# Performance work log

Measured on AMD Instinct MI355X. Metric: run time of the kernel, lower is better.

Reference implementation:

```python
import jax, jax.numpy as jnp
import numpy as np

IN, H = 24, 128


def _lstm_last(x, W_ih, W_hh, b_ih, b_hh):
    # x: [B, T, IN]. PyTorch gate order: i, f, g, o. Returns final hidden state [B, H].
    B = x.shape[0]
    b = b_ih + b_hh  # [4H]
    # Precompute input projections for all timesteps: [T, B, 4H]
    xg = jnp.einsum('bti,gi->tbg', x, W_ih) + b

    def step(carry, xg_t):
        h, c = carry
        gates = xg_t + h @ W_hh.T  # [B, 4H]
        i, f, g, o = jnp.split(gates, 4, axis=-1)
        i = jax.nn.sigmoid(i)
        f = jax.nn.sigmoid(f)
        g = jnp.tanh(g)
        o = jax.nn.sigmoid(o)
        c = f * c + i * g
        h = o * jnp.tanh(c)
        return (h, c), None

    h0 = jnp.zeros((B, H), x.dtype)
    (h, _), _ = jax.lax.scan(step, (h0, h0), xg)
    return h


def setup_inputs() -> dict:
    key = jax.random.key(0)
    ks = jax.random.split(key, 10)
    s_ih = 1.0 / np.sqrt(H)
    return {
        'x': jax.random.normal(ks[0], (1024, 512, IN), jnp.float32),
        'additional_input': jax.random.normal(ks[1], (1024, 2), jnp.float32),
        'W_ih': jax.random.uniform(ks[2], (4 * H, IN), jnp.float32, -s_ih, s_ih),
        'W_hh': jax.random.uniform(ks[3], (4 * H, H), jnp.float32, -s_ih, s_ih),
        'b_ih': jax.random.uniform(ks[4], (4 * H,), jnp.float32, -s_ih, s_ih),
        'b_hh': jax.random.uniform(ks[5], (4 * H,), jnp.float32, -s_ih, s_ih),
        'W1': jax.random.uniform(ks[6], (64, H + 2), jnp.float32, -1/np.sqrt(H + 2), 1/np.sqrt(H + 2)),
        'b1': jax.random.uniform(ks[7], (64,), jnp.float32, -1/np.sqrt(H + 2), 1/np.sqrt(H + 2)),
        'W2': jax.random.uniform(ks[8], (3, 64), jnp.float32, -1/8.0, 1/8.0),
        'b2': jax.random.uniform(ks[9], (3,), jnp.float32, -1/8.0, 1/8.0),
    }


def reference(x, additional_input, W_ih, W_hh, b_ih, b_hh, W1, b1, W2, b2):
    h_last = _lstm_last(x, W_ih, W_hh, b_ih, b_hh)  # [B, H]
    combined = jnp.concatenate([h_last, additional_input], axis=1)  # [B, H+2]
    # fc: Dropout (identity in eval) -> ReLU -> Linear -> Dropout -> ReLU -> Linear
    z = jax.nn.relu(combined) @ W1.T + b1
    out = jax.nn.relu(z) @ W2.T + b2  # [B, 3]
    return out
```

## Files before the change

### kernel.cpp

```cpp
#include <hip/hip_runtime.h>
#include <cstdint>
#include <cstddef>

#define TSTEPS 512
#define INP    24
#define HID    128
#define BB     4
#define NKT    5
#define VSTR   168
#define NTHR   576

typedef __attribute__((ext_vector_type(8))) _Float16 half8;
typedef __attribute__((ext_vector_type(4))) float f32x4;

__device__ __forceinline__ float rcp_f(float v) { return __builtin_amdgcn_rcpf(v); }
__device__ __forceinline__ float sigm_f(float v) {
    return rcp_f(1.0f + __expf(-v));
}
__device__ __forceinline__ float tanh_f(float v) {
    return 1.0f - 2.0f * rcp_f(1.0f + __expf(2.0f * v));
}
__device__ __forceinline__ unsigned pack2h(float a, float b) {
    union { _Float16 h[2]; unsigned u; } z;
    z.h[0] = (_Float16)a; z.h[1] = (_Float16)b;
    return z.u;
}
__device__ __forceinline__ float sel4(const f32x4 a, bool rb0, bool rb1) {
    const float lo = rb0 ? a[1] : a[0];
    const float hi = rb0 ? a[3] : a[2];
    return rb1 ? hi : lo;
}

__global__ __launch_bounds__(NTHR)
void lstm_fused(
    const float* __restrict__ x,
    const float* __restrict__ addin,
    const float* __restrict__ W_ih,
    const float* __restrict__ W_hh,
    const float* __restrict__ b_ih,
    const float* __restrict__ b_hh,
    const float* __restrict__ W1,
    const float* __restrict__ b1,
    const float* __restrict__ W2,
    const float* __restrict__ b2,
    float* __restrict__ out)
{
    __shared__ _Float16 v_s[2][BB * VSTR];
    __shared__ float z_s[BB][64];

    const int t    = threadIdx.x;
    const int lane = t & 63;
    const int wv   = t >> 6;
    const bool is_stage = (wv == 8);
    const int ncol = lane & 15;
    const int quad = lane >> 4;
    const int b0   = blockIdx.x * BB;
    const int bsel = ncol & 3;
    const bool rb0 = (ncol >> 2) & 1;
    const bool rb1 = (ncol >> 3) & 1;

    const int sb = lane / 12;
    const int kk = lane - sb * 12;
    const size_t xrow = (size_t)(b0 + (sb & 3)) * TSTEPS;

    for (int i = t; i < BB * VSTR; i += NTHR) {
        v_s[0][i] = (_Float16)0.0f; v_s[1][i] = (_Float16)0.0f;
    }
    __syncthreads();

    if (is_stage) {
        float2 xq = {0.f, 0.f};
        if (lane < 48) {
            const float2 x0 = *(const float2*)(x + (xrow + 0) * INP + kk * 2);
            const float2 x1 = *(const float2*)(x + (xrow + 1) * INP + kk * 2);
            *(unsigned*)&v_s[0][sb * VSTR + HID + kk * 2] = pack2h(x0.x, x0.y);
            *(unsigned*)&v_s[1][sb * VSTR + HID + kk * 2] = pack2h(x1.x, x1.y);
            xq = *(const float2*)(x + (xrow + 2) * INP + kk * 2);
        }
        __syncthreads();
        __syncthreads();
        for (int ts = 0; ts < TSTEPS; ++ts) {
            const int pb = ts & 1;
            if (lane < 48) {
                const int tsn = (ts + 3 < TSTEPS) ? ts + 3 : TSTEPS - 1;
                const float2 xn = *(const float2*)(x + (xrow + tsn) * INP + kk * 2);
                *(unsigned*)&v_s[pb][sb * VSTR + HID + kk * 2] = pack2h(xq.x, xq.y);
                xq = xn;
            }
            __syncthreads();
        }
    } else {
        half8 A_w[4][NKT];
        #pragma unroll
        for (int g = 0; g < 4; ++g) {
            const int row = g * HID + wv * 16 + ncol;
            #pragma unroll
            for (int kt = 0; kt < NKT; ++kt) {
                half8 frag;
                #pragma unroll
                for (int j = 0; j < 8; ++j) {
                    const int k = kt * 32 + quad * 8 + j;
                    float w = 0.0f;
                    if (k < HID)            w = W_hh[row * HID + k];
                    else if (k < HID + INP) w = W_ih[row * INP + (k - HID)];
                    frag[j] = (_Float16)w;
                }
                A_w[g][kt] = frag;
            }
        }
        f32x4 biasv[4];
        #pragma unroll
        for (int g = 0; g < 4; ++g) {
            #pragma unroll
            for (int r = 0; r < 4; ++r) {
                const int u = wv * 16 + quad * 4 + r;
                biasv[g][r] = b_ih[g * HID + u] + b_hh[g * HID + u];
            }
        }
        const int uj = wv * 16 + quad * 4 + (ncol >> 2);
        float c_reg = 0.0f;

        __syncthreads();

        half8 bxh = *(const half8*)(&v_s[0][0] + bsel * VSTR + HID + quad * 8);
        __syncthreads();

        #pragma unroll 2
        for (int ts = 0; ts < TSTEPS; ++ts) {
            const int pb = ts & 1, nb = pb ^ 1;
            const _Float16* vh = v_s[pb];

            const half8 bh0 = *(const half8*)(vh + bsel * VSTR + 0 * 32 + quad * 8);
            const half8 bh1 = *(const half8*)(vh + bsel * VSTR + 1 * 32 + quad * 8);
            const half8 bh2 = *(const half8*)(vh + bsel * VSTR + 2 * 32 + quad * 8);
            const half8 bh3 = *(const half8*)(vh + bsel * VSTR + 3 * 32 + quad * 8);
            const half8 bxn = *(const half8*)(&v_s[nb][0] + bsel * VSTR + HID + quad * 8);

            const f32x4 aci = __builtin_amdgcn_mfma_f32_16x16x32_f16(A_w[0][4], bxh, biasv[0], 0, 0, 0);
            const f32x4 acf = __builtin_amdgcn_mfma_f32_16x16x32_f16(A_w[1][4], bxh, biasv[1], 0, 0, 0);
            const f32x4 acg = __builtin_amdgcn_mfma_f32_16x16x32_f16(A_w[2][4], bxh, biasv[2], 0, 0, 0);
            const f32x4 aco = __builtin_amdgcn_mfma_f32_16x16x32_f16(A_w[3][4], bxh, biasv[3], 0, 0, 0);

            __builtin_amdgcn_s_setprio(1);
            f32x4 ai = __builtin_amdgcn_mfma_f32_16x16x32_f16(A_w[0][0], bh0, aci, 0, 0, 0);
            f32x4 af = __builtin_amdgcn_mfma_f32_16x16x32_f16(A_w[1][0], bh0, acf, 0, 0, 0);
            f32x4 ag = __builtin_amdgcn_mfma_f32_16x16x32_f16(A_w[2][0], bh0, acg, 0, 0, 0);
            f32x4 ao = __builtin_amdgcn_mfma_f32_16x16x32_f16(A_w[3][0], bh0, aco, 0, 0, 0);
            ai = __builtin_amdgcn_mfma_f32_16x16x32_f16(A_w[0][1], bh1, ai, 0, 0, 0);
            af = __builtin_amdgcn_mfma_f32_16x16x32_f16(A_w[1][1], bh1, af, 0, 0, 0);
            ag = __builtin_amdgcn_mfma_f32_16x16x32_f16(A_w[2][1], bh1, ag, 0, 0, 0);
            ao = __builtin_amdgcn_mfma_f32_16x16x32_f16(A_w[3][1], bh1, ao, 0, 0, 0);
            ai = __builtin_amdgcn_mfma_f32_16x16x32_f16(A_w[0][2], bh2, ai, 0, 0, 0);
            af = __builtin_amdgcn_mfma_f32_16x16x32_f16(A_w[1][2], bh2, af, 0, 0, 0);
            ag = __builtin_amdgcn_mfma_f32_16x16x32_f16(A_w[2][2], bh2, ag, 0, 0, 0);
            ao = __builtin_amdgcn_mfma_f32_16x16x32_f16(A_w[3][2], bh2, ao, 0, 0, 0);
            ai = __builtin_amdgcn_mfma_f32_16x16x32_f16(A_w[0][3], bh3, ai, 0, 0, 0);
            af = __builtin_amdgcn_mfma_f32_16x16x32_f16(A_w[1][3], bh3, af, 0, 0, 0);
            ag = __builtin_amdgcn_mfma_f32_16x16x32_f16(A_w[2][3], bh3, ag, 0, 0, 0);
            ao = __builtin_amdgcn_mfma_f32_16x16x32_f16(A_w[3][3], bh3, ao, 0, 0, 0);
            __builtin_amdgcn_s_setprio(0);

            const float si = sel4(ai, rb0, rb1);
            const float sf = sel4(af, rb0, rb1);
            const float sg = sel4(ag, rb0, rb1);
            const float so = sel4(ao, rb0, rb1);
            {
                const float gi = sigm_f(si);
                const float gf = sigm_f(sf);
                const float gg = tanh_f(sg);
                const float go = sigm_f(so);
                c_reg = gf * c_reg + gi * gg;
                const float h = go * tanh_f(c_reg);
                v_s[nb][bsel * VSTR + uj] = (_Float16)h;
            }

            bxh = bxn;

            __syncthreads();
        }
    }

    if (t < 64 * BB) {
        const int b = t >> 6, u = t & 63;
        const float* w = W1 + u * 130;
        float a = b1[u];
        #pragma unroll 16
        for (int k = 0; k < HID; ++k) {
            const float hv = (float)v_s[0][b * VSTR + k];
            a += fmaxf(hv, 0.0f) * w[k];
        }
        const float a0 = addin[(size_t)(b0 + b) * 2 + 0];
        const float a1 = addin[(size_t)(b0 + b) * 2 + 1];
        a += fmaxf(a0, 0.0f) * w[128] + fmaxf(a1, 0.0f) * w[129];
        z_s[b][u] = fmaxf(a, 0.0f);
    }
    __syncthreads();
    if (t < 3 * BB) {
        const int b = t / 3, o = t - 3 * b;
        const float* w = W2 + o * 64;
        float a = b2[o];
        #pragma unroll
        for (int k = 0; k < 64; ++k)
            a += z_s[b][k] * w[k];
        out[(size_t)(b0 + b) * 3 + o] = a;
    }
}

extern "C" void kernel_launch(void* const* d_in, const int* in_sizes, int n_in,
                              void* d_out, int out_size, void* d_ws, size_t ws_size,
                              hipStream_t stream) {
    const float* x     = (const float*)d_in[0];
    const float* addin = (const float*)d_in[1];
    const float* W_ih  = (const float*)d_in[2];
    const float* W_hh  = (const float*)d_in[3];
    const float* b_ih  = (const float*)d_in[4];
    const float* b_hh  = (const float*)d_in[5];
    const float* W1    = (const float*)d_in[6];
    const float* b1    = (const float*)d_in[7];
    const float* W2    = (const float*)d_in[8];
    const float* b2    = (const float*)d_in[9];
    float* outp        = (float*)d_out;

    const int B = in_sizes[0] / (TSTEPS * INP);
    const int grid = B / BB;

    lstm_fused<<<grid, NTHR, 0, stream>>>(x, addin, W_ih, W_hh, b_ih, b_hh,
                                          W1, b1, W2, b2, outp);
}
```

Measured before the change: 367.1 us.

## Preload entire x sequence into LDS and drop dedicated staging wavefront

Removes the separate staging wave that streamed x one timestep at a time into the double-buffered LDS vector. Instead all 512 timesteps of x for the block's 4 batch rows are converted to fp16 and loaded into a 128 KB LDS array before the recurrence. Every wave then reads its input fragment directly from that array. This cuts the block to 512 threads and takes global loads off the per-step critical path, at the cost of a large LDS footprint and an up-front load phase.

```diff
diff --git a/kernel.cpp b/kernel.cpp
--- a/kernel.cpp
+++ b/kernel.cpp
@@ -8,7 +8,7 @@
 #define BB     4
 #define NKT    5
 #define VSTR   168
-#define NTHR   576
+#define NTHR   512
 
 typedef __attribute__((ext_vector_type(8))) _Float16 half8;
 typedef __attribute__((ext_vector_type(4))) float f32x4;
@@ -45,13 +45,13 @@
     const float* __restrict__ b2,
     float* __restrict__ out)
 {
+    __shared__ _Float16 xc[TSTEPS][4][32];
     __shared__ _Float16 v_s[2][BB * VSTR];
     __shared__ float z_s[BB][64];
 
     const int t    = threadIdx.x;
     const int lane = t & 63;
     const int wv   = t >> 6;
-    const bool is_stage = (wv == 8);
     const int ncol = lane & 15;
     const int quad = lane >> 4;
     const int b0   = blockIdx.x * BB;
@@ -59,125 +59,109 @@
     const bool rb0 = (ncol >> 2) & 1;
     const bool rb1 = (ncol >> 3) & 1;
 
-    const int sb = lane / 12;
-    const int kk = lane - sb * 12;
-    const size_t xrow = (size_t)(b0 + (sb & 3)) * TSTEPS;
-
-    for (int i = t; i < BB * VSTR; i += NTHR) {
-        v_s[0][i] = (_Float16)0.0f; v_s[1][i] = (_Float16)0.0f;
+    half8 A_w[4][NKT];
+    #pragma unroll
+    for (int g = 0; g < 4; ++g) {
+        const int row = g * HID + wv * 16 + ncol;
+        #pragma unroll
+        for (int kt = 0; kt < NKT; ++kt) {
+            half8 frag;
+            #pragma unroll
+            for (int j = 0; j < 8; ++j) {
+                const int k = kt * 32 + quad * 8 + j;
+                float w = 0.0f;
+                if (k < HID)            w = W_hh[row * HID + k];
+                else if (k < HID + INP) w = W_ih[row * INP + (k - HID)];
+                frag[j] = (_Float16)w;
+            }
+            A_w[g][kt] = frag;
+        }
+    }
+    f32x4 biasv[4];
+    #pragma unroll
+    for (int g = 0; g < 4; ++g) {
+        #pragma unroll
+        for (int r = 0; r < 4; ++r) {
+            const int u = wv * 16 + quad * 4 + r;
+            biasv[g][r] = b_ih[g * HID + u] + b_hh[g * HID + u];
+        }
+    }
+    const int uj = wv * 16 + quad * 4 + (ncol >> 2);
+    float c_reg = 0.0f;
+
+    {
+        _Float16* vz = &v_s[0][0];
+        for (int i = t; i < 2 * BB * VSTR; i += NTHR) vz[i] = (_Float16)0.0f;
+    }
+    for (int idx = t; idx < 4 * TSTEPS * 16; idx += NTHR) {
+        const int kkp = idx & 15;
+        const int tsz = (idx >> 4) & (TSTEPS - 1);
+        const int bz  = idx >> 13;
+        unsigned val = 0u;
+        if (kkp < 12) {
+            const float2 xv = *(const float2*)(
+                x + ((size_t)(b0 + bz) * TSTEPS + tsz) * INP + kkp * 2);
+            val = pack2h(xv.x, xv.y);
+        }
+        *(unsigned*)&xc[tsz][bz][kkp * 2] = val;
     }
     __syncthreads();
 
-    if (is_stage) {
-        float2 xq = {0.f, 0.f};
-        if (lane < 48) {
-            const float2 x0 = *(const float2*)(x + (xrow + 0) * INP + kk * 2);
-            const float2 x1 = *(const float2*)(x + (xrow + 1) * INP + kk * 2);
-            *(unsigned*)&v_s[0][sb * VSTR + HID + kk * 2] = pack2h(x0.x, x0.y);
-            *(unsigned*)&v_s[1][sb * VSTR + HID + kk * 2] = pack2h(x1.x, x1.y);
-            xq = *(const float2*)(x + (xrow + 2) * INP + kk * 2);
-        }
+    half8 bxh = *(const half8*)&xc[0][bsel][quad * 8];
+
+    #pragma unroll 2
+    for (int ts = 0; ts < TSTEPS; ++ts) {
+        const int pb = ts & 1, nb = pb ^ 1;
+        const _Float16* vh = v_s[pb];
+
+        const half8 bh0 = *(const half8*)(vh + bsel * VSTR + 0 * 32 + quad * 8);
+        const half8 bh1 = *(const half8*)(vh + bsel * VSTR + 1 * 32 + quad * 8);
+        const half8 bh2 = *(const half8*)(vh + bsel * VSTR + 2 * 32 + quad * 8);
+        const half8 bh3 = *(const half8*)(vh + bsel * VSTR + 3 * 32 + quad * 8);
+        const int tsn = (ts + 1 < TSTEPS) ? ts + 1 : TSTEPS - 1;
+        const half8 bxn = *(const half8*)&xc[tsn][bsel][quad * 8];
+
+        const f32x4 acg = __builtin_amdgcn_mfma_f32_16x16x32_f16(A_w[2][4], bxh, biasv[2], 0, 0, 0);
+        const f32x4 aci = __builtin_amdgcn_mfma_f32_16x16x32_f16(A_w[0][4], bxh, biasv[0], 0, 0, 0);
+        const f32x4 acf = __builtin_amdgcn_mfma_f32_16x16x32_f16(A_w[1][4], bxh, biasv[1], 0, 0, 0);
+        const f32x4 aco = __builtin_amdgcn_mfma_f32_16x16x32_f16(A_w[3][4], bxh, biasv[3], 0, 0, 0);
+
+        __builtin_amdgcn_s_setprio(1);
+        f32x4 ag = __builtin_amdgcn_mfma_f32_16x16x32_f16(A_w[2][0], bh0, acg, 0, 0, 0);
+        f32x4 ai = __builtin_amdgcn_mfma_f32_16x16x32_f16(A_w[0][0], bh0, aci, 0, 0, 0);
+        f32x4 af = __builtin_amdgcn_mfma_f32_16x16x32_f16(A_w[1][0], bh0, acf, 0, 0, 0);
+        f32x4 ao = __builtin_amdgcn_mfma_f32_16x16x32_f16(A_w[3][0], bh0, aco, 0, 0, 0);
+        ag = __builtin_amdgcn_mfma_f32_16x16x32_f16(A_w[2][1], bh1, ag, 0, 0, 0);
+        ai = __builtin_amdgcn_mfma_f32_16x16x32_f16(A_w[0][1], bh1, ai, 0, 0, 0);
+        af = __builtin_amdgcn_mfma_f32_16x16x32_f16(A_w[1][1], bh1, af, 0, 0, 0);
+        ao = __builtin_amdgcn_mfma_f32_16x16x32_f16(A_w[3][1], bh1, ao, 0, 0, 0);
+        ag = __builtin_amdgcn_mfma_f32_16x16x32_f16(A_w[2][2], bh2, ag, 0, 0, 0);
+        ai = __builtin_amdgcn_mfma_f32_16x16x32_f16(A_w[0][2], bh2, ai, 0, 0, 0);
+        af = __builtin_amdgcn_mfma_f32_16x16x32_f16(A_w[1][2], bh2, af, 0, 0, 0);
+        ao = __builtin_amdgcn_mfma_f32_16x16x32_f16(A_w[3][2], bh2, ao, 0, 0, 0);
+        ag = __builtin_amdgcn_mfma_f32_16x16x32_f16(A_w[2][3], bh3, ag, 0, 0, 0);
+        ai = __builtin_amdgcn_mfma_f32_16x16x32_f16(A_w[0][3], bh3, ai, 0, 0, 0);
+        af = __builtin_amdgcn_mfma_f32_16x16x32_f16(A_w[1][3], bh3, af, 0, 0, 0);
+        ao = __builtin_amdgcn_mfma_f32_16x16x32_f16(A_w[3][3], bh3, ao, 0, 0, 0);
+        __builtin_amdgcn_s_setprio(0);
+
+        const float sg = sel4(ag, rb0, rb1);
+        const float si = sel4(ai, rb0, rb1);
+        const float sf = sel4(af, rb0, rb1);
+        const float so = sel4(ao, rb0, rb1);
+        {
+            const float gg = tanh_f(sg);
+            const float gi = sigm_f(si);
+            const float gf = sigm_f(sf);
+            const float go = sigm_f(so);
+            c_reg = gf * c_reg + gi * gg;
+            const float h = go * tanh_f(c_reg);
+            v_s[nb][bsel * VSTR + uj] = (_Float16)h;
+        }
+
+        bxh = bxn;
+
         __syncthreads();
-        __syncthreads();
-        for (int ts = 0; ts < TSTEPS; ++ts) {
-            const int pb = ts & 1;
-            if (lane < 48) {
-                const int tsn = (ts + 3 < TSTEPS) ? ts + 3 : TSTEPS - 1;
-                const float2 xn = *(const float2*)(x + (xrow + tsn) * INP + kk * 2);
-                *(unsigned*)&v_s[pb][sb * VSTR + HID + kk * 2] = pack2h(xq.x, xq.y);
-                xq = xn;
-            }
-            __syncthreads();
-        }
-    } else {
-        half8 A_w[4][NKT];
-        #pragma unroll
-        for (int g = 0; g < 4; ++g) {
-            const int row = g * HID + wv * 16 + ncol;
-            #pragma unroll
-            for (int kt = 0; kt < NKT; ++kt) {
-                half8 frag;
-                #pragma unroll
-                for (int j = 0; j < 8; ++j) {
-                    const int k = kt * 32 + quad * 8 + j;
-                    float w = 0.0f;
-                    if (k < HID)            w = W_hh[row * HID + k];
-                    else if (k < HID + INP) w = W_ih[row * INP + (k - HID)];
-                    frag[j] = (_Float16)w;
-                }
-                A_w[g][kt] = frag;
-            }
-        }
-        f32x4 biasv[4];
-        #pragma unroll
-        for (int g = 0; g < 4; ++g) {
-            #pragma unroll
-            for (int r = 0; r < 4; ++r) {
-                const int u = wv * 16 + quad * 4 + r;
-                biasv[g][r] = b_ih[g * HID + u] + b_hh[g * HID + u];
-            }
-        }
-        const int uj = wv * 16 + quad * 4 + (ncol >> 2);
-        float c_reg = 0.0f;
-
-        __syncthreads();
-
-        half8 bxh = *(const half8*)(&v_s[0][0] + bsel * VSTR + HID + quad * 8);
-        __syncthreads();
-
-        #pragma unroll 2
-        for (int ts = 0; ts < TSTEPS; ++ts) {
-            const int pb = ts & 1, nb = pb ^ 1;
-            const _Float16* vh = v_s[pb];
-
-            const half8 bh0 = *(const half8*)(vh + bsel * VSTR + 0 * 32 + quad * 8);
-            const half8 bh1 = *(const half8*)(vh + bsel * VSTR + 1 * 32 + quad * 8);
-            const half8 bh2 = *(const half8*)(vh + bsel * VSTR + 2 * 32 + quad * 8);
-            const half8 bh3 = *(const half8*)(vh + bsel * VSTR + 3 * 32 + quad * 8);
-            const half8 bxn = *(const half8*)(&v_s[nb][0] + bsel * VSTR + HID + quad * 8);
-
-            const f32x4 aci = __builtin_amdgcn_mfma_f32_16x16x32_f16(A_w[0][4], bxh, biasv[0], 0, 0, 0);
-            const f32x4 acf = __builtin_amdgcn_mfma_f32_16x16x32_f16(A_w[1][4], bxh, biasv[1], 0, 0, 0);
-            const f32x4 acg = __builtin_amdgcn_mfma_f32_16x16x32_f16(A_w[2][4], bxh, biasv[2], 0, 0, 0);
-            const f32x4 aco = __builtin_amdgcn_mfma_f32_16x16x32_f16(A_w[3][4], bxh, biasv[3], 0, 0, 0);
-
-            __builtin_amdgcn_s_setprio(1);
-            f32x4 ai = __builtin_amdgcn_mfma_f32_16x16x32_f16(A_w[0][0], bh0, aci, 0, 0, 0);
-            f32x4 af = __builtin_amdgcn_mfma_f32_16x16x32_f16(A_w[1][0], bh0, acf, 0, 0, 0);
-            f32x4 ag = __builtin_amdgcn_mfma_f32_16x16x32_f16(A_w[2][0], bh0, acg, 0, 0, 0);
-            f32x4 ao = __builtin_amdgcn_mfma_f32_16x16x32_f16(A_w[3][0], bh0, aco, 0, 0, 0);
-            ai = __builtin_amdgcn_mfma_f32_16x16x32_f16(A_w[0][1], bh1, ai, 0, 0, 0);
-            af = __builtin_amdgcn_mfma_f32_16x16x32_f16(A_w[1][1], bh1, af, 0, 0, 0);
-            ag = __builtin_amdgcn_mfma_f32_16x16x32_f16(A_w[2][1], bh1, ag, 0, 0, 0);
-            ao = __builtin_amdgcn_mfma_f32_16x16x32_f16(A_w[3][1], bh1, ao, 0, 0, 0);
-            ai = __builtin_amdgcn_mfma_f32_16x16x32_f16(A_w[0][2], bh2, ai, 0, 0, 0);
-            af = __builtin_amdgcn_mfma_f32_16x16x32_f16(A_w[1][2], bh2, af, 0, 0, 0);
-            ag = __builtin_amdgcn_mfma_f32_16x16x32_f16(A_w[2][2], bh2, ag, 0, 0, 0);
-            ao = __builtin_amdgcn_mfma_f32_16x16x32_f16(A_w[3][2], bh2, ao, 0, 0, 0);
-            ai = __builtin_amdgcn_mfma_f32_16x16x32_f16(A_w[0][3], bh3, ai, 0, 0, 0);
-            af = __builtin_amdgcn_mfma_f32_16x16x32_f16(A_w[1][3], bh3, af, 0, 0, 0);
-            ag = __builtin_amdgcn_mfma_f32_16x16x32_f16(A_w[2][3], bh3, ag, 0, 0, 0);
-            ao = __builtin_amdgcn_mfma_f32_16x16x32_f16(A_w[3][3], bh3, ao, 0, 0, 0);
-            __builtin_amdgcn_s_setprio(0);
-
-            const float si = sel4(ai, rb0, rb1);
-            const float sf = sel4(af, rb0, rb1);
-            const float sg = sel4(ag, rb0, rb1);
-            const float so = sel4(ao, rb0, rb1);
-            {
-                const float gi = sigm_f(si);
-                const float gf = sigm_f(sf);
-                const float gg = tanh_f(sg);
-                const float go = sigm_f(so);
-                c_reg = gf * c_reg + gi * gg;
-                const float h = go * tanh_f(c_reg);
-                v_s[nb][bsel * VSTR + uj] = (_Float16)h;
-            }
-
-            bxh = bxn;
-
-            __syncthreads();
-        }
     }
 
     if (t < 64 * BB) {
```

New measurement: 373.2 us. No clear change (+1.7%).
